# Performance work log

Hardware: AMD Instinct MI355X
Metric: run time of the kernel (lower is better)

## Reference

```python
import jax, jax.numpy as jnp
import numpy as np

H = 8
SPLIT = 1
# deterministic stand-in for random.shuffle(range(8)) in the original
_PERM = np.random.RandomState(0).permutation(H)
SERIES_IDX = jnp.asarray(_PERM[SPLIT:])  # 7 heads
CROSS_IDX = jnp.asarray(_PERM[:SPLIT])   # 1 head


def setup_inputs() -> dict:
    key = jax.random.key(0)
    ks = jax.random.split(key, 5)
    B, L, E = 8, 1024, 64
    shp = (B, L, H, E)
    return {
        "queries": jax.random.normal(ks[0], shp, dtype=jnp.float32),
        "keys": jax.random.normal(ks[1], shp, dtype=jnp.float32),
        "keysT": jax.random.normal(ks[2], shp, dtype=jnp.float32),
        "values": jax.random.normal(ks[3], shp, dtype=jnp.float32),
        "valuesT": jax.random.normal(ks[4], shp, dtype=jnp.float32),
    }


def reference(queries, keys, keysT, values, valuesT):
    B, L, _, E = queries.shape
    scale = 1.0 / jnp.sqrt(jnp.asarray(E, dtype=queries.dtype))
    neg_inf = jnp.asarray(-jnp.inf, dtype=queries.dtype)

    # head split (gather along head dim)
    sq = queries[:, :, SERIES_IDX]   # [B,L,7,E]
    sk = keys[:, :, SERIES_IDX]      # [B,S,7,E]
    sv = values[:, :, SERIES_IDX]    # [B,S,7,D]
    cq = queries[:, :, CROSS_IDX]    # [B,L,1,E]
    ckT = keysT[:, :, CROSS_IDX]     # [B,C,1,E]
    cvT = valuesT[:, :, CROSS_IDX]   # [B,C,1,D]

    # causal mask: True above the diagonal -> disallowed
    causal = jnp.triu(jnp.ones((L, L), dtype=bool), k=1)  # [L,L]

    # series branch
    scores = jnp.einsum('blne,bsne->bnls', sq, sk)  # [B,7,L,S]
    scores = jnp.where(causal[None, None], neg_inf, scores * scale)
    series = jax.nn.softmax(scores, axis=-1)
    V = jnp.einsum('bhls,bshd->blhd', series, sv)   # [B,L,7,D]

    # cross branch
    cscores = jnp.einsum('blme,bcme->bmlc', cq, ckT)  # [B,1,L,C]
    cscores = jnp.where(causal[None, None], neg_inf, cscores * scale)
    crosses = jax.nn.softmax(cscores, axis=-1)
    V_cross = jnp.einsum('bhlc,bchd->blhd', crosses, cvT)  # [B,L,1,D]

    return jnp.concatenate([V, V_cross], axis=2)  # [B,L,8,D]
```

## Files before the change

### kernel.cpp

```cpp
#include <hip/hip_runtime.h>
#include <math.h>

#define Lq 1024
#define Hq 8
#define Eq 64
#define LDW 72
#define PTW 40

#define SRC_HEAD_PACKED 0x64503712u

typedef __bf16 bf16_t;
typedef __bf16 bf16x8 __attribute__((ext_vector_type(8)));
typedef __bf16 bf16x4 __attribute__((ext_vector_type(4)));
typedef float floatx4 __attribute__((ext_vector_type(4)));

__device__ __forceinline__ bf16x8 cvt8(const float4 a, const float4 b) {
    bf16x8 r;
    r[0] = (bf16_t)a.x; r[1] = (bf16_t)a.y; r[2] = (bf16_t)a.z; r[3] = (bf16_t)a.w;
    r[4] = (bf16_t)b.x; r[5] = (bf16_t)b.y; r[6] = (bf16_t)b.z; r[7] = (bf16_t)b.w;
    return r;
}

__global__ __launch_bounds__(512, 4)
void attn_mfma(const float* __restrict__ Q, const float* __restrict__ Ks,
               const float* __restrict__ KTs, const float* __restrict__ Vs,
               const float* __restrict__ VTs, float* __restrict__ out) {
    const int slot = blockIdx.x;
    const int b    = blockIdx.y;
    const int p    = blockIdx.z;
    const int h    = (SRC_HEAD_PACKED >> (slot * 4)) & 0xF;
    const float* __restrict__ Kp = (slot == 7) ? KTs : Ks;
    const float* __restrict__ Vp = (slot == 7) ? VTs : Vs;
    const int pA = p, pB = 15 - p;

    const int tid  = threadIdx.x;
    const int wv   = tid >> 6;
    const int lane = tid & 63;
    const int ln16 = lane & 15;
    const int quad = lane >> 4;
    const int wq   = wv & 3;
    const int kh   = wv >> 2;

    __shared__ alignas(16) unsigned short smem[64 * LDW * 2 + 8 * 16 * PTW];
    unsigned short (*k_lds)[LDW]  = (unsigned short (*)[LDW])smem;
    unsigned short (*vt_lds)[LDW] = (unsigned short (*)[LDW])(smem + 64 * LDW);
    unsigned short (*pt)[PTW]     = (unsigned short (*)[PTW])(smem + 2 * 64 * LDW + wv * 16 * PTW);

    const float qs = 0.125f * 1.44269504f;
    bf16x8 qfA[2], qfB[2];
    {
        const int rA = pA * 64 + wq * 16 + ln16;
        const int rB = pB * 64 + wq * 16 + ln16;
        const float* qa = Q + (((size_t)b * Lq + rA) * Hq + h) * Eq + quad * 8;
        const float* qb = Q + (((size_t)b * Lq + rB) * Hq + h) * Eq + quad * 8;
        #pragma unroll
        for (int ec = 0; ec < 2; ++ec) {
            float4 f0 = ((const float4*)(qa + ec * 32))[0];
            float4 f1 = ((const float4*)(qa + ec * 32))[1];
            float4 g0 = ((const float4*)(qb + ec * 32))[0];
            float4 g1 = ((const float4*)(qb + ec * 32))[1];
            f0.x*=qs; f0.y*=qs; f0.z*=qs; f0.w*=qs; f1.x*=qs; f1.y*=qs; f1.z*=qs; f1.w*=qs;
            g0.x*=qs; g0.y*=qs; g0.z*=qs; g0.w*=qs; g1.x*=qs; g1.y*=qs; g1.z*=qs; g1.w*=qs;
            qfA[ec] = cvt8(f0, f1);
            qfB[ec] = cvt8(g0, g1);
        }
    }

    floatx4 OA[4], OB[4];
    #pragma unroll
    for (int i = 0; i < 4; ++i) { OA[i] = (floatx4){0,0,0,0}; OB[i] = (floatx4){0,0,0,0}; }
    float mA = -1e30f, lA = 0.f, mB = -1e30f, lB = 0.f;

    float4 kq[2];
    float  vq[8];
    const int kj = tid >> 3, kc = (tid & 7) * 8;
    const int vd = tid & 63, vk = wv * 8;

    auto load_tile = [&](int kt) {
        const float* kb = Kp + (((size_t)b * Lq + kt * 64 + kj) * Hq + h) * Eq + kc;
        kq[0] = ((const float4*)kb)[0]; kq[1] = ((const float4*)kb)[1];
        const float* vb = Vp + (((size_t)b * Lq + kt * 64 + vk) * Hq + h) * Eq + vd;
        #pragma unroll
        for (int i = 0; i < 8; ++i) vq[i] = vb[(size_t)i * (Hq * Eq)];
    };

    auto process = [&](const bf16x8* qf, const bf16x8 kf[2][2], const bf16x8 vf[4],
                       floatx4* O, float& m, float& l, bool diag) {
        floatx4 s[2];
        #pragma unroll
        for (int nc = 0; nc < 2; ++nc) {
            floatx4 acc = (floatx4){0,0,0,0};
            acc = __builtin_amdgcn_mfma_f32_16x16x32_bf16(kf[nc][0], qf[0], acc, 0, 0, 0);
            acc = __builtin_amdgcn_mfma_f32_16x16x32_bf16(kf[nc][1], qf[1], acc, 0, 0, 0);
            s[nc] = acc;
        }
        if (diag) {
            const int rin = wq * 16 + ln16;
            #pragma unroll
            for (int nc = 0; nc < 2; ++nc)
                #pragma unroll
                for (int r = 0; r < 4; ++r)
                    if (kh * 32 + nc * 16 + quad * 4 + r > rin) s[nc][r] = -INFINITY;
        }
        float mn = s[0][0];
        #pragma unroll
        for (int nc = 0; nc < 2; ++nc)
            #pragma unroll
            for (int r = 0; r < 4; ++r) mn = fmaxf(mn, s[nc][r]);
        mn = fmaxf(mn, __shfl_xor(mn, 16, 64));
        mn = fmaxf(mn, __shfl_xor(mn, 32, 64));
        mn = fmaxf(mn, m);
        const float alpha = __builtin_amdgcn_exp2f(m - mn);
        m = mn;
        float ps = 0.f;
        float pv[2][4];
        #pragma unroll
        for (int nc = 0; nc < 2; ++nc)
            #pragma unroll
            for (int r = 0; r < 4; ++r) { pv[nc][r] = __builtin_amdgcn_exp2f(s[nc][r] - mn); ps += pv[nc][r]; }
        ps += __shfl_xor(ps, 16, 64);
        ps += __shfl_xor(ps, 32, 64);
        l = l * alpha + ps;
        #pragma unroll
        for (int dc = 0; dc < 4; ++dc) O[dc] *= alpha;
        #pragma unroll
        for (int nc = 0; nc < 2; ++nc) {
            bf16x4 pk;
            pk[0] = (bf16_t)pv[nc][0]; pk[1] = (bf16_t)pv[nc][1];
            pk[2] = (bf16_t)pv[nc][2]; pk[3] = (bf16_t)pv[nc][3];
            *(bf16x4*)&pt[ln16][nc * 16 + quad * 4] = pk;
        }
        bf16x8 pf = *(const bf16x8*)&pt[ln16][quad * 8];
        #pragma unroll
        for (int dc = 0; dc < 4; ++dc)
            O[dc] = __builtin_amdgcn_mfma_f32_16x16x32_bf16(vf[dc], pf, O[dc], 0, 0, 0);
    };

    load_tile(0);
    for (int kt = 0; kt <= pB; ++kt) {
        __syncthreads();
        *(bf16x8*)&k_lds[kj][kc] = cvt8(kq[0], kq[1]);
        {
            const float4* vq4 = (const float4*)vq;
            *(bf16x8*)&vt_lds[vd][vk] = cvt8(vq4[0], vq4[1]);
        }
        if (kt < pB) load_tile(kt + 1);
        __syncthreads();

        bf16x8 kf[2][2], vf[4];
        #pragma unroll
        for (int c = 0; c < 2; ++c) {
            kf[c][0] = *(const bf16x8*)&k_lds[(kh * 2 + c) * 16 + ln16][quad * 8];
            kf[c][1] = *(const bf16x8*)&k_lds[(kh * 2 + c) * 16 + ln16][32 + quad * 8];
        }
        #pragma unroll
        for (int c = 0; c < 4; ++c)
            vf[c] = *(const bf16x8*)&vt_lds[c * 16 + ln16][kh * 32 + quad * 8];

        if (kt <= pA) process(qfA, kf, vf, OA, mA, lA, kt == pA);
        process(qfB, kf, vf, OB, mB, lB, kt == pB);
    }

    __syncthreads();
    float* mbuf = (float*)smem;

    if (kh) {
        float* dst = mbuf + (wq * 64 + lane) * 18;
        #pragma unroll
        for (int dc = 0; dc < 4; ++dc) {
            *(float2*)(dst + dc * 4)     = make_float2(OA[dc][0], OA[dc][1]);
            *(float2*)(dst + dc * 4 + 2) = make_float2(OA[dc][2], OA[dc][3]);
        }
        dst[16] = mA; dst[17] = lA;
    }
    __syncthreads();
    if (!kh) {
        const float* src = mbuf + (wq * 64 + lane) * 18;
        const float m1 = src[16], l1 = src[17];
        const float mm = fmaxf(mA, m1);
        const float a0 = __builtin_amdgcn_exp2f(mA - mm);
        const float a1 = __builtin_amdgcn_exp2f(m1 - mm);
        const float inv = 1.0f / (lA * a0 + l1 * a1);
        const int row = pA * 64 + wq * 16 + ln16;
        float* op = out + (((size_t)b * Lq + row) * Hq + slot) * Eq + quad * 4;
        #pragma unroll
        for (int dc = 0; dc < 4; ++dc) {
            float4 o;
            o.x = (OA[dc][0] * a0 + src[dc * 4 + 0] * a1) * inv;
            o.y = (OA[dc][1] * a0 + src[dc * 4 + 1] * a1) * inv;
            o.z = (OA[dc][2] * a0 + src[dc * 4 + 2] * a1) * inv;
            o.w = (OA[dc][3] * a0 + src[dc * 4 + 3] * a1) * inv;
            *(float4*)(op + dc * 16) = o;
        }
    }
    __syncthreads();

    if (kh) {
        float* dst = mbuf + (wq * 64 + lane) * 18;
        #pragma unroll
        for (int dc = 0; dc < 4; ++dc) {
            *(float2*)(dst + dc * 4)     = make_float2(OB[dc][0], OB[dc][1]);
            *(float2*)(dst + dc * 4 + 2) = make_float2(OB[dc][2], OB[dc][3]);
        }
        dst[16] = mB; dst[17] = lB;
    }
    __syncthreads();
    if (!kh) {
        const float* src = mbuf + (wq * 64 + lane) * 18;
        const float m1 = src[16], l1 = src[17];
        const float mm = fmaxf(mB, m1);
        const float a0 = __builtin_amdgcn_exp2f(mB - mm);
        const float a1 = __builtin_amdgcn_exp2f(m1 - mm);
        const float inv = 1.0f / (lB * a0 + l1 * a1);
        const int row = pB * 64 + wq * 16 + ln16;
        float* op = out + (((size_t)b * Lq + row) * Hq + slot) * Eq + quad * 4;
        #pragma unroll
        for (int dc = 0; dc < 4; ++dc) {
            float4 o;
            o.x = (OB[dc][0] * a0 + src[dc * 4 + 0] * a1) * inv;
            o.y = (OB[dc][1] * a0 + src[dc * 4 + 1] * a1) * inv;
            o.z = (OB[dc][2] * a0 + src[dc * 4 + 2] * a1) * inv;
            o.w = (OB[dc][3] * a0 + src[dc * 4 + 3] * a1) * inv;
            *(float4*)(op + dc * 16) = o;
        }
    }
}

extern "C" void kernel_launch(void* const* d_in, const int* in_sizes, int n_in,
                              void* d_out, int out_size, void* d_ws, size_t ws_size,
                              hipStream_t stream) {
    const float* queries = (const float*)d_in[0];
    const float* keys    = (const float*)d_in[1];
    const float* keysT   = (const float*)d_in[2];
    const float* values  = (const float*)d_in[3];
    const float* valuesT = (const float*)d_in[4];
    float* out = (float*)d_out;

    dim3 grid(Hq, 8, 8);
    dim3 block(512);
    attn_mfma<<<grid, block, 0, stream>>>(queries, keys, keysT, values, valuesT, out);
}
```

Baseline: 138.7 us.

## Split paired query tiles across 1024-thread blocks with double-buffered K/V staging

The block grows from 512 to 1024 threads. Each half of the block (8 waves) now owns one of the two paired query tiles (pA or pB), where before every wave processed both tiles serially. K/V tiles are now double-buffered in LDS with a two-tile-ahead global prefetch, which removes one barrier per iteration, and each thread loads half as much data. The cost is that the pA half sits idle at barriers once it finishes its shorter causal range. The larger block also raises LDS and register pressure under the new launch bounds.

```diff
diff --git a/kernel.cpp b/kernel.cpp
--- a/kernel.cpp
+++ b/kernel.cpp
@@ -6,6 +6,9 @@
 #define Eq 64
 #define LDW 72
 #define PTW 40
+#define KV_SH (64 * LDW)
+#define BUF_SH (2 * KV_SH)
+#define PT_OFS (2 * BUF_SH)
 
 #define SRC_HEAD_PACKED 0x64503712u
 
@@ -20,8 +23,13 @@
     r[4] = (bf16_t)b.x; r[5] = (bf16_t)b.y; r[6] = (bf16_t)b.z; r[7] = (bf16_t)b.w;
     return r;
 }
-
-__global__ __launch_bounds__(512, 4)
+__device__ __forceinline__ bf16x4 cvt4(const float4 a) {
+    bf16x4 r;
+    r[0] = (bf16_t)a.x; r[1] = (bf16_t)a.y; r[2] = (bf16_t)a.z; r[3] = (bf16_t)a.w;
+    return r;
+}
+
+__global__ __launch_bounds__(1024, 8)
 void attn_mfma(const float* __restrict__ Q, const float* __restrict__ Ks,
                const float* __restrict__ KTs, const float* __restrict__ Vs,
                const float* __restrict__ VTs, float* __restrict__ out) {
@@ -39,188 +47,155 @@
     const int ln16 = lane & 15;
     const int quad = lane >> 4;
     const int wq   = wv & 3;
-    const int kh   = wv >> 2;
-
-    __shared__ alignas(16) unsigned short smem[64 * LDW * 2 + 8 * 16 * PTW];
-    unsigned short (*k_lds)[LDW]  = (unsigned short (*)[LDW])smem;
-    unsigned short (*vt_lds)[LDW] = (unsigned short (*)[LDW])(smem + 64 * LDW);
-    unsigned short (*pt)[PTW]     = (unsigned short (*)[PTW])(smem + 2 * 64 * LDW + wv * 16 * PTW);
+    const int kh   = (wv >> 2) & 1;
+    const int tb   = wv >> 3;
+    const int pT   = tb ? pB : pA;
+
+    __shared__ alignas(16) unsigned short smem[PT_OFS + 16 * 16 * PTW];
+    unsigned short* ptp = smem + PT_OFS + wv * 16 * PTW;
 
     const float qs = 0.125f * 1.44269504f;
-    bf16x8 qfA[2], qfB[2];
+    bf16x8 qf[2];
     {
-        const int rA = pA * 64 + wq * 16 + ln16;
-        const int rB = pB * 64 + wq * 16 + ln16;
-        const float* qa = Q + (((size_t)b * Lq + rA) * Hq + h) * Eq + quad * 8;
-        const float* qb = Q + (((size_t)b * Lq + rB) * Hq + h) * Eq + quad * 8;
+        const int r = pT * 64 + wq * 16 + ln16;
+        const float* qa = Q + (((size_t)b * Lq + r) * Hq + h) * Eq + quad * 8;
         #pragma unroll
         for (int ec = 0; ec < 2; ++ec) {
             float4 f0 = ((const float4*)(qa + ec * 32))[0];
             float4 f1 = ((const float4*)(qa + ec * 32))[1];
-            float4 g0 = ((const float4*)(qb + ec * 32))[0];
-            float4 g1 = ((const float4*)(qb + ec * 32))[1];
-            f0.x*=qs; f0.y*=qs; f0.z*=qs; f0.w*=qs; f1.x*=qs; f1.y*=qs; f1.z*=qs; f1.w*=qs;
-            g0.x*=qs; g0.y*=qs; g0.z*=qs; g0.w*=qs; g1.x*=qs; g1.y*=qs; g1.z*=qs; g1.w*=qs;
-            qfA[ec] = cvt8(f0, f1);
-            qfB[ec] = cvt8(g0, g1);
-        }
-    }
-
-    floatx4 OA[4], OB[4];
+            f0.x*=qs; f0.y*=qs; f0.z*=qs; f0.w*=qs;
+            f1.x*=qs; f1.y*=qs; f1.z*=qs; f1.w*=qs;
+            qf[ec] = cvt8(f0, f1);
+        }
+    }
+
+    floatx4 O[4];
     #pragma unroll
-    for (int i = 0; i < 4; ++i) { OA[i] = (floatx4){0,0,0,0}; OB[i] = (floatx4){0,0,0,0}; }
-    float mA = -1e30f, lA = 0.f, mB = -1e30f, lB = 0.f;
-
-    float4 kq[2];
-    float  vq[8];
-    const int kj = tid >> 3, kc = (tid & 7) * 8;
-    const int vd = tid & 63, vk = wv * 8;
+    for (int i = 0; i < 4; ++i) O[i] = (floatx4){0, 0, 0, 0};
+    float m = -1e30f, l = 0.f;
+
+    float4 kq;
+    float  vq[4];
+    const int kj = tid >> 4, kc = (tid & 15) * 4;
+    const int vd = lane,     vkg = (tid >> 6) * 4;
 
     auto load_tile = [&](int kt) {
-        const float* kb = Kp + (((size_t)b * Lq + kt * 64 + kj) * Hq + h) * Eq + kc;
-        kq[0] = ((const float4*)kb)[0]; kq[1] = ((const float4*)kb)[1];
-        const float* vb = Vp + (((size_t)b * Lq + kt * 64 + vk) * Hq + h) * Eq + vd;
-        #pragma unroll
-        for (int i = 0; i < 8; ++i) vq[i] = vb[(size_t)i * (Hq * Eq)];
+        kq = *(const float4*)(Kp + (((size_t)b * Lq + kt * 64 + kj) * Hq + h) * Eq + kc);
+        const float* vb = Vp + (((size_t)b * Lq + kt * 64 + vkg) * Hq + h) * Eq + vd;
+        #pragma unroll
+        for (int i = 0; i < 4; ++i) vq[i] = vb[(size_t)i * (Hq * Eq)];
     };
-
-    auto process = [&](const bf16x8* qf, const bf16x8 kf[2][2], const bf16x8 vf[4],
-                       floatx4* O, float& m, float& l, bool diag) {
-        floatx4 s[2];
-        #pragma unroll
-        for (int nc = 0; nc < 2; ++nc) {
-            floatx4 acc = (floatx4){0,0,0,0};
-            acc = __builtin_amdgcn_mfma_f32_16x16x32_bf16(kf[nc][0], qf[0], acc, 0, 0, 0);
-            acc = __builtin_amdgcn_mfma_f32_16x16x32_bf16(kf[nc][1], qf[1], acc, 0, 0, 0);
-            s[nc] = acc;
-        }
-        if (diag) {
-            const int rin = wq * 16 + ln16;
+    auto stage = [&](int buf) {
+        unsigned short* base = smem + buf * BUF_SH;
+        *(bf16x4*)&base[kj * LDW + kc] = cvt4(kq);
+        float4 vv; vv.x = vq[0]; vv.y = vq[1]; vv.z = vq[2]; vv.w = vq[3];
+        *(bf16x4*)&base[KV_SH + vd * LDW + vkg] = cvt4(vv);
+    };
+
+    load_tile(0);
+    stage(0);
+    load_tile(1);
+
+    for (int kt = 0; kt <= pB; ++kt) {
+        __syncthreads();
+        if (kt <= pT) {
+            const unsigned short* base = smem + (kt & 1) * BUF_SH;
+            bf16x8 kf[2][2], vf[4];
+            #pragma unroll
+            for (int c = 0; c < 2; ++c) {
+                kf[c][0] = *(const bf16x8*)&base[((kh * 2 + c) * 16 + ln16) * LDW + quad * 8];
+                kf[c][1] = *(const bf16x8*)&base[((kh * 2 + c) * 16 + ln16) * LDW + 32 + quad * 8];
+            }
+            #pragma unroll
+            for (int c = 0; c < 4; ++c)
+                vf[c] = *(const bf16x8*)&base[KV_SH + (c * 16 + ln16) * LDW + kh * 32 + quad * 8];
+
+            floatx4 s[2];
+            #pragma unroll
+            for (int nc = 0; nc < 2; ++nc) {
+                floatx4 acc = (floatx4){0, 0, 0, 0};
+                acc = __builtin_amdgcn_mfma_f32_16x16x32_bf16(kf[nc][0], qf[0], acc, 0, 0, 0);
+                acc = __builtin_amdgcn_mfma_f32_16x16x32_bf16(kf[nc][1], qf[1], acc, 0, 0, 0);
+                s[nc] = acc;
+            }
+            if (kt == pT) {
+                const int rin = wq * 16 + ln16;
+                #pragma unroll
+                for (int nc = 0; nc < 2; ++nc)
+                    #pragma unroll
+                    for (int r = 0; r < 4; ++r)
+                        if (kh * 32 + nc * 16 + quad * 4 + r > rin) s[nc][r] = -INFINITY;
+            }
+            float mn = s[0][0];
             #pragma unroll
             for (int nc = 0; nc < 2; ++nc)
                 #pragma unroll
-                for (int r = 0; r < 4; ++r)
-                    if (kh * 32 + nc * 16 + quad * 4 + r > rin) s[nc][r] = -INFINITY;
-        }
-        float mn = s[0][0];
-        #pragma unroll
-        for (int nc = 0; nc < 2; ++nc)
-            #pragma unroll
-            for (int r = 0; r < 4; ++r) mn = fmaxf(mn, s[nc][r]);
-        mn = fmaxf(mn, __shfl_xor(mn, 16, 64));
-        mn = fmaxf(mn, __shfl_xor(mn, 32, 64));
-        mn = fmaxf(mn, m);
-        const float alpha = __builtin_amdgcn_exp2f(m - mn);
-        m = mn;
-        float ps = 0.f;
-        float pv[2][4];
-        #pragma unroll
-        for (int nc = 0; nc < 2; ++nc)
-            #pragma unroll
-            for (int r = 0; r < 4; ++r) { pv[nc][r] = __builtin_amdgcn_exp2f(s[nc][r] - mn); ps += pv[nc][r]; }
-        ps += __shfl_xor(ps, 16, 64);
-        ps += __shfl_xor(ps, 32, 64);
-        l = l * alpha + ps;
-        #pragma unroll
-        for (int dc = 0; dc < 4; ++dc) O[dc] *= alpha;
-        #pragma unroll
-        for (int nc = 0; nc < 2; ++nc) {
-            bf16x4 pk;
-            pk[0] = (bf16_t)pv[nc][0]; pk[1] = (bf16_t)pv[nc][1];
-            pk[2] = (bf16_t)pv[nc][2]; pk[3] = (bf16_t)pv[nc][3];
-            *(bf16x4*)&pt[ln16][nc * 16 + quad * 4] = pk;
-        }
-        bf16x8 pf = *(const bf16x8*)&pt[ln16][quad * 8];
-        #pragma unroll
-        for (int dc = 0; dc < 4; ++dc)
-            O[dc] = __builtin_amdgcn_mfma_f32_16x16x32_bf16(vf[dc], pf, O[dc], 0, 0, 0);
-    };
-
-    load_tile(0);
-    for (int kt = 0; kt <= pB; ++kt) {
-        __syncthreads();
-        *(bf16x8*)&k_lds[kj][kc] = cvt8(kq[0], kq[1]);
-        {
-            const float4* vq4 = (const float4*)vq;
-            *(bf16x8*)&vt_lds[vd][vk] = cvt8(vq4[0], vq4[1]);
-        }
-        if (kt < pB) load_tile(kt + 1);
-        __syncthreads();
-
-        bf16x8 kf[2][2], vf[4];
-        #pragma unroll
-        for (int c = 0; c < 2; ++c) {
-            kf[c][0] = *(const bf16x8*)&k_lds[(kh * 2 + c) * 16 + ln16][quad * 8];
-            kf[c][1] = *(const bf16x8*)&k_lds[(kh * 2 + c) * 16 + ln16][32 + quad * 8];
-        }
-        #pragma unroll
-        for (int c = 0; c < 4; ++c)
-            vf[c] = *(const bf16x8*)&vt_lds[c * 16 + ln16][kh * 32 + quad * 8];
-
-        if (kt <= pA) process(qfA, kf, vf, OA, mA, lA, kt == pA);
-        process(qfB, kf, vf, OB, mB, lB, kt == pB);
+                for (int r = 0; r < 4; ++r) mn = fmaxf(mn, s[nc][r]);
+            mn = fmaxf(mn, __shfl_xor(mn, 16, 64));
+            mn = fmaxf(mn, __shfl_xor(mn, 32, 64));
+            mn = fmaxf(mn, m);
+            const float alpha = __builtin_amdgcn_exp2f(m - mn);
+            m = mn;
+            float ps = 0.f;
+            float pv[2][4];
+            #pragma unroll
+            for (int nc = 0; nc < 2; ++nc)
+                #pragma unroll
+                for (int r = 0; r < 4; ++r) {
+                    pv[nc][r] = __builtin_amdgcn_exp2f(s[nc][r] - mn);
+                    ps += pv[nc][r];
+                }
+            ps += __shfl_xor(ps, 16, 64);
+            ps += __shfl_xor(ps, 32, 64);
+            l = l * alpha + ps;
+            #pragma unroll
+            for (int dc = 0; dc < 4; ++dc) O[dc] *= alpha;
+            #pragma unroll
+            for (int nc = 0; nc < 2; ++nc) {
+                bf16x4 pk;
+                pk[0] = (bf16_t)pv[nc][0]; pk[1] = (bf16_t)pv[nc][1];
+                pk[2] = (bf16_t)pv[nc][2]; pk[3] = (bf16_t)pv[nc][3];
+                *(bf16x4*)&ptp[ln16 * PTW + nc * 16 + quad * 4] = pk;
+            }
+            bf16x8 pf = *(const bf16x8*)&ptp[ln16 * PTW + quad * 8];
+            #pragma unroll
+            for (int dc = 0; dc < 4; ++dc)
+                O[dc] = __builtin_amdgcn_mfma_f32_16x16x32_bf16(vf[dc], pf, O[dc], 0, 0, 0);
+        }
+        if (kt < pB) {
+            stage((kt + 1) & 1);
+            if (kt + 1 < pB) load_tile(kt + 2);
+        }
     }
 
     __syncthreads();
-    float* mbuf = (float*)smem;
-
+    float* mb = (float*)smem + tb * 4608;
     if (kh) {
-        float* dst = mbuf + (wq * 64 + lane) * 18;
+        float* dst = mb + (wq * 64 + lane) * 18;
         #pragma unroll
         for (int dc = 0; dc < 4; ++dc) {
-            *(float2*)(dst + dc * 4)     = make_float2(OA[dc][0], OA[dc][1]);
-            *(float2*)(dst + dc * 4 + 2) = make_float2(OA[dc][2], OA[dc][3]);
-        }
-        dst[16] = mA; dst[17] = lA;
+            *(float2*)(dst + dc * 4)     = make_float2(O[dc][0], O[dc][1]);
+            *(float2*)(dst + dc * 4 + 2) = make_float2(O[dc][2], O[dc][3]);
+        }
+        dst[16] = m; dst[17] = l;
     }
     __syncthreads();
     if (!kh) {
-        const float* src = mbuf + (wq * 64 + lane) * 18;
+        const float* src = mb + (wq * 64 + lane) * 18;
         const float m1 = src[16], l1 = src[17];
-        const float mm = fmaxf(mA, m1);
-        const float a0 = __builtin_amdgcn_exp2f(mA - mm);
+        const float mm = fmaxf(m, m1);
+        const float a0 = __builtin_amdgcn_exp2f(m - mm);
         const float a1 = __builtin_amdgcn_exp2f(m1 - mm);
-        const float inv = 1.0f / (lA * a0 + l1 * a1);
-        const int row = pA * 64 + wq * 16 + ln16;
+        const float inv = 1.0f / (l * a0 + l1 * a1);
+        const int row = pT * 64 + wq * 16 + ln16;
         float* op = out + (((size_t)b * Lq + row) * Hq + slot) * Eq + quad * 4;
         #pragma unroll
         for (int dc = 0; dc < 4; ++dc) {
             float4 o;
-            o.x = (OA[dc][0] * a0 + src[dc * 4 + 0] * a1) * inv;
-            o.y = (OA[dc][1] * a0 + src[dc * 4 + 1] * a1) * inv;
-            o.z = (OA[dc][2] * a0 + src[dc * 4 + 2] * a1) * inv;
-            o.w = (OA[dc][3] * a0 + src[dc * 4 + 3] * a1) * inv;
-            *(float4*)(op + dc * 16) = o;
-        }
-    }
-    __syncthreads();
-
-    if (kh) {
-        float* dst = mbuf + (wq * 64 + lane) * 18;
-        #pragma unroll
-        for (int dc = 0; dc < 4; ++dc) {
-            *(float2*)(dst + dc * 4)     = make_float2(OB[dc][0], OB[dc][1]);
-            *(float2*)(dst + dc * 4 + 2) = make_float2(OB[dc][2], OB[dc][3]);
-        }
-        dst[16] = mB; dst[17] = lB;
-    }
-    __syncthreads();
-    if (!kh) {
-        const float* src = mbuf + (wq * 64 + lane) * 18;
-        const float m1 = src[16], l1 = src[17];
-        const float mm = fmaxf(mB, m1);
-        const float a0 = __builtin_amdgcn_exp2f(mB - mm);
-        const float a1 = __builtin_amdgcn_exp2f(m1 - mm);
-        const float inv = 1.0f / (lB * a0 + l1 * a1);
-        const int row = pB * 64 + wq * 16 + ln16;
-        float* op = out + (((size_t)b * Lq + row) * Hq + slot) * Eq + quad * 4;
-        #pragma unroll
-        for (int dc = 0; dc < 4; ++dc) {
-            float4 o;
-            o.x = (OB[dc][0] * a0 + src[dc * 4 + 0] * a1) * inv;
-            o.y = (OB[dc][1] * a0 + src[dc * 4 + 1] * a1) * inv;
-            o.z = (OB[dc][2] * a0 + src[dc * 4 + 2] * a1) * inv;
-            o.w = (OB[dc][3] * a0 + src[dc * 4 + 3] * a1) * inv;
+            o.x = (O[dc][0] * a0 + src[dc * 4 + 0] * a1) * inv;
+            o.y = (O[dc][1] * a0 + src[dc * 4 + 1] * a1) * inv;
+            o.z = (O[dc][2] * a0 + src[dc * 4 + 2] * a1) * inv;
+            o.w = (O[dc][3] * a0 + src[dc * 4 + 3] * a1) * inv;
             *(float4*)(op + dc * 16) = o;
         }
     }
@@ -237,6 +212,6 @@
     float* out = (float*)d_out;
 
     dim3 grid(Hq, 8, 8);
-    dim3 block(512);
+    dim3 block(1024);
     attn_mfma<<<grid, block, 0, stream>>>(queries, keys, keysT, values, valuesT, out);
 }
```

After: 220.3 us. 58.9% more time.
